# Kernel tuning notes

Measured on AMD Instinct MI355X. Metric: run time of the kernel, lower is better.

Reference implementation:

```python
import jax, jax.numpy as jnp
import numpy as np

B, N, IN_F = 16, 1024, 256
HEADS, OUT_F = 4, 64
NEG_SLOPE = 0.2
CLAMP_MIN = -1e9
MASK_VAL = -9e15


def setup_inputs() -> dict:
    key = jax.random.key(0)
    k1, k2, k3, k4 = jax.random.split(key, 4)
    x = jax.random.normal(k1, (B, N, IN_F), dtype=jnp.float32)
    adj = jax.random.randint(k2, (B, N, N), 0, 2, dtype=jnp.int32)
    # Linear weight, stored as (in, heads*out) so y = x @ W (xavier-uniform scale)
    lim_w = float(np.sqrt(6.0 / (IN_F + HEADS * OUT_F)))
    W = jax.random.uniform(k3, (IN_F, HEADS * OUT_F), dtype=jnp.float32,
                           minval=-lim_w, maxval=lim_w)
    lim_a = float(np.sqrt(6.0 / (2 * OUT_F + HEADS)))
    a = jax.random.uniform(k4, (2 * OUT_F, HEADS), dtype=jnp.float32,
                           minval=-lim_a, maxval=lim_a)
    return {"x": x, "adj": adj, "W": W, "a": a}


def reference(x, adj, W, a):
    Bs, Ns, _ = x.shape
    # Projection: (B,N,H,D)
    h = (x @ W).reshape(Bs, Ns, HEADS, OUT_F)
    # cat([h_i, h_j]) . a == h_i . a_src + h_j . a_dst  (exact same math, no O(N^2*2D) tensor)
    a_src, a_dst = a[:OUT_F], a[OUT_F:]          # each (D, H)
    s_src = jnp.einsum('bnhd,dh->bnh', h, a_src)  # score contribution of node i
    s_dst = jnp.einsum('bnhd,dh->bnh', h, a_dst)  # score contribution of node j
    e = jax.nn.leaky_relu(s_src[:, :, None, :] + s_dst[:, None, :, :],
                          negative_slope=NEG_SLOPE)  # (B,N,N,H)
    # match original: subtract unmasked row max, clamp, then mask, then softmax over j
    e = e - jnp.max(e, axis=2, keepdims=True)
    e = jnp.maximum(e, CLAMP_MIN)
    att = jnp.where(adj[..., None] > 0, e, MASK_VAL)
    att = jax.nn.softmax(att, axis=2)
    h_prime = jnp.einsum('bijh,bjhd->bihd', att, h)  # (B,N,H,D)
    return h_prime.reshape(Bs, Ns, HEADS * OUT_F)
```

## Files before the change

### kernel.cpp

```cpp
#include <hip/hip_runtime.h>
#include <hip/hip_bf16.h>

#define B_   16
#define N_   1024
#define INF_ 256
#define NH_  4
#define HD_  256
#define L2E  1.4426950408889634f

typedef __attribute__((ext_vector_type(8))) short short8;
typedef __attribute__((ext_vector_type(4))) float f32x4;

__device__ __forceinline__ float bf2f(unsigned short u) {
    union { unsigned int i; float f; } v; v.i = ((unsigned int)u) << 16; return v.f;
}
__device__ __forceinline__ unsigned short f2bf(float f) {
    union { float f; unsigned int i; } v; v.f = f;
    unsigned int x = v.i;
    return (unsigned short)((x + 0x7fffu + ((x >> 16) & 1u)) >> 16);
}

__global__ __launch_bounds__(256) void k_prepw(const float* __restrict__ W,
                                               unsigned short* __restrict__ wswz)
{
    int slot = blockIdx.x * 256 + threadIdx.x;
    int kstep = slot >> 10;
    int nt    = (slot >> 6) & 15;
    int lane  = slot & 63;
    int k0 = kstep * 32 + (lane >> 4) * 8;
    int n  = nt * 16 + (lane & 15);
    ushort4 o0, o1;
    o0.x = f2bf(W[(k0 + 0) * HD_ + n]);
    o0.y = f2bf(W[(k0 + 1) * HD_ + n]);
    o0.z = f2bf(W[(k0 + 2) * HD_ + n]);
    o0.w = f2bf(W[(k0 + 3) * HD_ + n]);
    o1.x = f2bf(W[(k0 + 4) * HD_ + n]);
    o1.y = f2bf(W[(k0 + 5) * HD_ + n]);
    o1.z = f2bf(W[(k0 + 6) * HD_ + n]);
    o1.w = f2bf(W[(k0 + 7) * HD_ + n]);
    *(ushort4*)&wswz[(long)slot * 8]     = o0;
    *(ushort4*)&wswz[(long)slot * 8 + 4] = o1;
}

__global__ __launch_bounds__(256) void k_gemm_h(
    const float* __restrict__ x, const float* __restrict__ a,
    const unsigned short* __restrict__ wswz,
    unsigned short* __restrict__ hswz,
    float* __restrict__ ssrc, float* __restrict__ sdst)
{
    __shared__ unsigned short xls[16][264];
    int t = threadIdx.x;
    int blk = blockIdx.x;
    int row0 = blk * 16;
    int b  = blk >> 6;
    int n0 = row0 & 1023;

    {
        int sr = t >> 4, sc = (t & 15) * 16;
        const float* xp = x + (long)(row0 + sr) * INF_ + sc;
        float4 v0 = ((const float4*)xp)[0];
        float4 v1 = ((const float4*)xp)[1];
        float4 v2 = ((const float4*)xp)[2];
        float4 v3 = ((const float4*)xp)[3];
        ushort4 u0 = {f2bf(v0.x), f2bf(v0.y), f2bf(v0.z), f2bf(v0.w)};
        ushort4 u1 = {f2bf(v1.x), f2bf(v1.y), f2bf(v1.z), f2bf(v1.w)};
        ushort4 u2 = {f2bf(v2.x), f2bf(v2.y), f2bf(v2.z), f2bf(v2.w)};
        ushort4 u3 = {f2bf(v3.x), f2bf(v3.y), f2bf(v3.z), f2bf(v3.w)};
        *(ushort4*)&xls[sr][sc]      = u0;
        *(ushort4*)&xls[sr][sc + 4]  = u1;
        *(ushort4*)&xls[sr][sc + 8]  = u2;
        *(ushort4*)&xls[sr][sc + 12] = u3;
    }
    __syncthreads();

    int wave = t >> 6, lane = t & 63, quad = lane >> 4, l15 = lane & 15;
    f32x4 acc[4];
    #pragma unroll
    for (int i = 0; i < 4; i++) acc[i] = (f32x4){0.f, 0.f, 0.f, 0.f};

    #pragma unroll
    for (int ks = 0; ks < 8; ks++) {
        short8 af = *(const short8*)&xls[l15][ks * 32 + quad * 8];
        #pragma unroll
        for (int nt = 0; nt < 4; nt++) {
            short8 bf = *(const short8*)(wswz +
                ((long)((ks * 16 + wave * 4 + nt) * 64 + lane)) * 8);
            acc[nt] = __builtin_amdgcn_mfma_f32_16x16x32_bf16(af, bf, acc[nt], 0, 0, 0);
        }
    }

    int q0 = (quad & 1) * 4;
    int qd = ((row0 & 31) + quad * 4) >> 3;
    long bj32 = row0 >> 5;
    #pragma unroll
    for (int nt = 0; nt < 4; nt++) {
        int dg = wave * 4 + nt;
        long idx8 = (bj32 * 16 + dg) * 64 + qd * 16 + l15;
        ushort4 o = {f2bf(acc[nt][0]), f2bf(acc[nt][1]),
                     f2bf(acc[nt][2]), f2bf(acc[nt][3])};
        *(ushort4*)&hswz[idx8 * 8 + q0] = o;
    }

    float as_[4], ad_[4];
    #pragma unroll
    for (int nt = 0; nt < 4; nt++) {
        int d = nt * 16 + l15;
        as_[nt] = a[d * NH_ + wave];
        ad_[nt] = a[(64 + d) * NH_ + wave];
    }
    #pragma unroll
    for (int r = 0; r < 4; r++) {
        float ps = acc[0][r] * as_[0] + acc[1][r] * as_[1]
                 + acc[2][r] * as_[2] + acc[3][r] * as_[3];
        float pd = acc[0][r] * ad_[0] + acc[1][r] * ad_[1]
                 + acc[2][r] * ad_[2] + acc[3][r] * ad_[3];
        #pragma unroll
        for (int m = 1; m < 16; m <<= 1) {
            ps += __shfl_xor(ps, m);
            pd += __shfl_xor(pd, m);
        }
        if (l15 == 0) {
            int row = n0 + quad * 4 + r;
            ssrc[((long)b * NH_ + wave) * N_ + row] = ps;
            sdst[((long)b * NH_ + wave) * N_ + row] = pd;
        }
    }
}

__global__ __launch_bounds__(256) void k_maxdst(const float* __restrict__ sdst,
                                                float* __restrict__ mx)
{
    int bh = blockIdx.x;
    int t  = threadIdx.x;
    const float* p = sdst + (long)bh * N_;
    float m = -1e30f;
    for (int i = t; i < N_; i += 256) m = fmaxf(m, p[i]);
    #pragma unroll
    for (int s = 1; s < 64; s <<= 1) m = fmaxf(m, __shfl_xor(m, s));
    __shared__ float sm[4];
    if ((t & 63) == 0) sm[t >> 6] = m;
    __syncthreads();
    if (t == 0) mx[bh] = fmaxf(fmaxf(sm[0], sm[1]), fmaxf(sm[2], sm[3]));
}

__global__ __launch_bounds__(512) void k_attn(
    const int* __restrict__ adj, const unsigned short* __restrict__ hswz,
    const float* __restrict__ ssrc, const float* __restrict__ sdst,
    const float* __restrict__ mxd, float* __restrict__ out)
{
    __shared__ float ss_s[4][32], m_s[4][32], den_l[4][32];

    int t = threadIdx.x;
    int b     = blockIdx.x >> 5;
    int itile = blockIdx.x & 31;
    int i0 = itile * 32;
    int wave = t >> 6, lane = t & 63, quad = lane >> 4, l15 = lane & 15;
    int hh = wave & 3, it = wave >> 2;

    if (t < 128) {
        int h = t >> 5, i = t & 31;
        float ss = ssrc[((long)b * NH_ + h) * N_ + i0 + i] * L2E;
        float mxv = mxd[b * NH_ + h] * L2E;
        ss_s[h][i] = ss;
        float e = ss + mxv;
        m_s[h][i] = fmaxf(e, 0.2f * e);
    }
    __syncthreads();

    int irow = it * 16 + l15;
    float ssi = ss_s[hh][irow];
    float mi  = m_s[hh][irow];
    const float* sdp = sdst + ((long)b * NH_ + hh) * N_;
    const int* adjrow = adj + ((long)b * N_ + i0 + irow) * N_;

    f32x4 acc[4];
    #pragma unroll
    for (int i = 0; i < 4; i++) acc[i] = (f32x4){0.f, 0.f, 0.f, 0.f};
    float den = 0.f;

    #pragma unroll 2
    for (int jc = 0; jc < 32; jc++) {
        int j0 = jc * 32;
        float4 s0 = *(const float4*)(sdp + j0 + quad * 8);
        float4 s1 = *(const float4*)(sdp + j0 + quad * 8 + 4);
        int4  a0 = *(const int4*)(adjrow + j0 + quad * 8);
        int4  a1 = *(const int4*)(adjrow + j0 + quad * 8 + 4);
        float sv[8] = {s0.x, s0.y, s0.z, s0.w, s1.x, s1.y, s1.z, s1.w};
        int   av[8] = {a0.x, a0.y, a0.z, a0.w, a1.x, a1.y, a1.z, a1.w};
        short8 af;
        #pragma unroll
        for (int q = 0; q < 8; q++) {
            float e  = ssi + sv[q] * L2E;
            float lr = fmaxf(e, 0.2f * e);
            float w  = (av[q] > 0) ? __builtin_exp2f(lr - mi) : 0.f;
            unsigned short ub = f2bf(w);
            den += bf2f(ub);
            af[q] = (short)ub;
        }
        long base8 = ((long)(b * 32) + jc) * 1024;
        #pragma unroll
        for (int idt = 0; idt < 4; idt++) {
            int dg = hh * 4 + idt;
            short8 bf = *(const short8*)(hswz + (base8 + dg * 64 + lane) * 8);
            acc[idt] = __builtin_amdgcn_mfma_f32_16x16x32_bf16(af, bf, acc[idt], 0, 0, 0);
        }
    }

    den += __shfl_xor(den, 16);
    den += __shfl_xor(den, 32);
    if (quad == 0) den_l[hh][irow] = den;
    __syncthreads();

    #pragma unroll
    for (int idt = 0; idt < 4; idt++) {
        #pragma unroll
        for (int r = 0; r < 4; r++) {
            int ir = it * 16 + quad * 4 + r;
            float inv = 1.0f / den_l[hh][ir];
            out[((long)b * N_ + i0 + ir) * HD_ + hh * 64 + idt * 16 + l15] =
                acc[idt][r] * inv;
        }
    }
}

extern "C" void kernel_launch(void* const* d_in, const int* in_sizes, int n_in,
                              void* d_out, int out_size, void* d_ws, size_t ws_size,
                              hipStream_t stream) {
    const float* x   = (const float*)d_in[0];
    const int*   adj = (const int*)d_in[1];
    const float* W   = (const float*)d_in[2];
    const float* a   = (const float*)d_in[3];
    float* out = (float*)d_out;

    unsigned short* hswz = (unsigned short*)d_ws;
    unsigned short* wswz = hswz + (long)B_ * N_ * HD_;
    float* ssrc = (float*)(wswz + INF_ * HD_);
    float* sdst = ssrc + (long)B_ * NH_ * N_;
    float* mxd  = sdst + (long)B_ * NH_ * N_;

    k_prepw<<<32, 256, 0, stream>>>(W, wswz);
    k_gemm_h<<<1024, 256, 0, stream>>>(x, a, wswz, hswz, ssrc, sdst);
    k_maxdst<<<64, 256, 0, stream>>>(sdst, mxd);
    k_attn<<<512, 512, 0, stream>>>(adj, hswz, ssrc, sdst, mxd, out);
}
```

Before: 176.0 us.

## Split attention over j halves, bit-pack adjacency, drop row-max pass

Adds a kernel that packs the int32 adjacency matrix into bitmasks. The attention kernel then reads one mask word per lane instead of int4 loads inside the loop. The attention kernel uses 16-row tiles with the j range split across two wave groups, and the partial accumulators are merged through shared memory. This doubles the block count to improve parallelism. The max-over-destination kernel and the max subtraction are removed, on the basis that softmax is shift-invariant, and the log2(e) scaling is folded into the projection kernel. The projection GEMM now keeps the W fragments in registers and processes two row tiles per block with a swizzled LDS layout. Without the max shift, exp2 can overflow if scores are large, and the packing kernel still reads the whole adjacency matrix.

```diff
diff --git a/kernel.cpp b/kernel.cpp
--- a/kernel.cpp
+++ b/kernel.cpp
@@ -42,64 +42,55 @@
     *(ushort4*)&wswz[(long)slot * 8 + 4] = o1;
 }
 
-__global__ __launch_bounds__(256) void k_gemm_h(
+__global__ __launch_bounds__(256) void k_pack(const int* __restrict__ adj,
+                                              unsigned int* __restrict__ pb)
+{
+    int g = blockIdx.x * 256 + threadIdx.x;
+    int gw   = g & 7;
+    int lane = (g >> 3) & 63;
+    int it   = (g >> 9) & 63;
+    int b    = g >> 15;
+    int row  = it * 16 + (lane & 15);
+    int quad = lane >> 4;
+    const int* ar = adj + ((long)(b * N_ + row) << 10);
+    unsigned int u = 0;
+    #pragma unroll
+    for (int jl = 0; jl < 4; jl++) {
+        int j0 = (gw * 4 + jl) * 32 + quad * 8;
+        int4 a0 = *(const int4*)(ar + j0);
+        int4 a1 = *(const int4*)(ar + j0 + 4);
+        u |= ((unsigned)a0.x) << (jl * 8 + 0);
+        u |= ((unsigned)a0.y) << (jl * 8 + 1);
+        u |= ((unsigned)a0.z) << (jl * 8 + 2);
+        u |= ((unsigned)a0.w) << (jl * 8 + 3);
+        u |= ((unsigned)a1.x) << (jl * 8 + 4);
+        u |= ((unsigned)a1.y) << (jl * 8 + 5);
+        u |= ((unsigned)a1.z) << (jl * 8 + 6);
+        u |= ((unsigned)a1.w) << (jl * 8 + 7);
+    }
+    pb[g] = u;
+}
+
+__global__ __launch_bounds__(256, 2) void k_gemm_h(
     const float* __restrict__ x, const float* __restrict__ a,
     const unsigned short* __restrict__ wswz,
     unsigned short* __restrict__ hswz,
     float* __restrict__ ssrc, float* __restrict__ sdst)
 {
-    __shared__ unsigned short xls[16][264];
+    __shared__ unsigned short xf[2][4096];
     int t = threadIdx.x;
-    int blk = blockIdx.x;
-    int row0 = blk * 16;
-    int b  = blk >> 6;
-    int n0 = row0 & 1023;
-
-    {
-        int sr = t >> 4, sc = (t & 15) * 16;
-        const float* xp = x + (long)(row0 + sr) * INF_ + sc;
-        float4 v0 = ((const float4*)xp)[0];
-        float4 v1 = ((const float4*)xp)[1];
-        float4 v2 = ((const float4*)xp)[2];
-        float4 v3 = ((const float4*)xp)[3];
-        ushort4 u0 = {f2bf(v0.x), f2bf(v0.y), f2bf(v0.z), f2bf(v0.w)};
-        ushort4 u1 = {f2bf(v1.x), f2bf(v1.y), f2bf(v1.z), f2bf(v1.w)};
-        ushort4 u2 = {f2bf(v2.x), f2bf(v2.y), f2bf(v2.z), f2bf(v2.w)};
-        ushort4 u3 = {f2bf(v3.x), f2bf(v3.y), f2bf(v3.z), f2bf(v3.w)};
-        *(ushort4*)&xls[sr][sc]      = u0;
-        *(ushort4*)&xls[sr][sc + 4]  = u1;
-        *(ushort4*)&xls[sr][sc + 8]  = u2;
-        *(ushort4*)&xls[sr][sc + 12] = u3;
-    }
-    __syncthreads();
-
     int wave = t >> 6, lane = t & 63, quad = lane >> 4, l15 = lane & 15;
-    f32x4 acc[4];
-    #pragma unroll
-    for (int i = 0; i < 4; i++) acc[i] = (f32x4){0.f, 0.f, 0.f, 0.f};
-
-    #pragma unroll
-    for (int ks = 0; ks < 8; ks++) {
-        short8 af = *(const short8*)&xls[l15][ks * 32 + quad * 8];
-        #pragma unroll
-        for (int nt = 0; nt < 4; nt++) {
-            short8 bf = *(const short8*)(wswz +
+
+    short8 bw[8][4];
+    #pragma unroll
+    for (int ks = 0; ks < 8; ks++)
+        #pragma unroll
+        for (int nt = 0; nt < 4; nt++)
+            bw[ks][nt] = *(const short8*)(wswz +
                 ((long)((ks * 16 + wave * 4 + nt) * 64 + lane)) * 8);
-            acc[nt] = __builtin_amdgcn_mfma_f32_16x16x32_bf16(af, bf, acc[nt], 0, 0, 0);
-        }
-    }
-
-    int q0 = (quad & 1) * 4;
-    int qd = ((row0 & 31) + quad * 4) >> 3;
-    long bj32 = row0 >> 5;
-    #pragma unroll
-    for (int nt = 0; nt < 4; nt++) {
-        int dg = wave * 4 + nt;
-        long idx8 = (bj32 * 16 + dg) * 64 + qd * 16 + l15;
-        ushort4 o = {f2bf(acc[nt][0]), f2bf(acc[nt][1]),
-                     f2bf(acc[nt][2]), f2bf(acc[nt][3])};
-        *(ushort4*)&hswz[idx8 * 8 + q0] = o;
-    }
+
+    int sr = t >> 4, c = t & 15;
+    int ks0 = c >> 1, qA = (c & 1) * 2;
 
     float as_[4], ad_[4];
     #pragma unroll
@@ -108,117 +99,169 @@
         as_[nt] = a[d * NH_ + wave];
         ad_[nt] = a[(64 + d) * NH_ + wave];
     }
-    #pragma unroll
-    for (int r = 0; r < 4; r++) {
-        float ps = acc[0][r] * as_[0] + acc[1][r] * as_[1]
-                 + acc[2][r] * as_[2] + acc[3][r] * as_[3];
-        float pd = acc[0][r] * ad_[0] + acc[1][r] * ad_[1]
-                 + acc[2][r] * ad_[2] + acc[3][r] * ad_[3];
-        #pragma unroll
-        for (int m = 1; m < 16; m <<= 1) {
-            ps += __shfl_xor(ps, m);
-            pd += __shfl_xor(pd, m);
-        }
-        if (l15 == 0) {
-            int row = n0 + quad * 4 + r;
-            ssrc[((long)b * NH_ + wave) * N_ + row] = ps;
-            sdst[((long)b * NH_ + wave) * N_ + row] = pd;
-        }
-    }
-}
-
-__global__ __launch_bounds__(256) void k_maxdst(const float* __restrict__ sdst,
-                                                float* __restrict__ mx)
-{
-    int bh = blockIdx.x;
+
+    for (int s = 0; s < 2; s++) {
+        int row0 = (blockIdx.x * 2 + s) * 16;
+        int b  = row0 >> 10;
+        int n0 = row0 & 1023;
+        unsigned short* xb = &xf[s][0];
+
+        {
+            const float* xp = x + (long)(row0 + sr) * INF_ + c * 16;
+            float4 v0 = ((const float4*)xp)[0];
+            float4 v1 = ((const float4*)xp)[1];
+            float4 v2 = ((const float4*)xp)[2];
+            float4 v3 = ((const float4*)xp)[3];
+            short8 u0, u1;
+            u0[0] = (short)f2bf(v0.x); u0[1] = (short)f2bf(v0.y);
+            u0[2] = (short)f2bf(v0.z); u0[3] = (short)f2bf(v0.w);
+            u0[4] = (short)f2bf(v1.x); u0[5] = (short)f2bf(v1.y);
+            u0[6] = (short)f2bf(v1.z); u0[7] = (short)f2bf(v1.w);
+            u1[0] = (short)f2bf(v2.x); u1[1] = (short)f2bf(v2.y);
+            u1[2] = (short)f2bf(v2.z); u1[3] = (short)f2bf(v2.w);
+            u1[4] = (short)f2bf(v3.x); u1[5] = (short)f2bf(v3.y);
+            u1[6] = (short)f2bf(v3.z); u1[7] = (short)f2bf(v3.w);
+            int sw = (ks0 & 1) << 2;
+            int i1 = ks0 * 64 + (((qA    ) * 16 + sr) ^ sw);
+            int i2 = ks0 * 64 + (((qA + 1) * 16 + sr) ^ sw);
+            *(short8*)(xb + i1 * 8) = u0;
+            *(short8*)(xb + i2 * 8) = u1;
+        }
+        __syncthreads();
+
+        f32x4 acc[4];
+        #pragma unroll
+        for (int i = 0; i < 4; i++) acc[i] = (f32x4){0.f, 0.f, 0.f, 0.f};
+
+        #pragma unroll
+        for (int ks = 0; ks < 8; ks++) {
+            short8 af = *(const short8*)(xb +
+                (ks * 64 + (lane ^ ((ks & 1) << 2))) * 8);
+            #pragma unroll
+            for (int nt = 0; nt < 4; nt++)
+                acc[nt] = __builtin_amdgcn_mfma_f32_16x16x32_bf16(af, bw[ks][nt], acc[nt], 0, 0, 0);
+        }
+
+        int q0 = (quad & 1) * 4;
+        int qd = ((row0 & 31) >> 3) + (quad >> 1);
+        long bj32 = row0 >> 5;
+        #pragma unroll
+        for (int nt = 0; nt < 4; nt++) {
+            int dg = wave * 4 + nt;
+            long idx8 = (bj32 * 16 + dg) * 64 + qd * 16 + l15;
+            ushort4 o = {f2bf(acc[nt][0]), f2bf(acc[nt][1]),
+                         f2bf(acc[nt][2]), f2bf(acc[nt][3])};
+            *(ushort4*)&hswz[idx8 * 8 + q0] = o;
+        }
+
+        #pragma unroll
+        for (int r = 0; r < 4; r++) {
+            float ps = acc[0][r] * as_[0] + acc[1][r] * as_[1]
+                     + acc[2][r] * as_[2] + acc[3][r] * as_[3];
+            float pd = acc[0][r] * ad_[0] + acc[1][r] * ad_[1]
+                     + acc[2][r] * ad_[2] + acc[3][r] * ad_[3];
+            #pragma unroll
+            for (int m = 1; m < 16; m <<= 1) {
+                ps += __shfl_xor(ps, m);
+                pd += __shfl_xor(pd, m);
+            }
+            if (l15 == 0) {
+                int row = n0 + quad * 4 + r;
+                ssrc[((long)b * NH_ + wave) * N_ + row] = ps * L2E;
+                sdst[((long)b * NH_ + wave) * N_ + row] = pd * L2E;
+            }
+        }
+    }
+}
+
+__global__ __launch_bounds__(512, 6) void k_attn(
+    const unsigned int* __restrict__ pb, const unsigned short* __restrict__ hswz,
+    const float* __restrict__ ssrc, const float* __restrict__ sdst,
+    float* __restrict__ out)
+{
+    __shared__ float ss_s[4][16];
+    __shared__ float accb[4][64][20];
+    __shared__ float denb[4][64];
+
     int t  = threadIdx.x;
-    const float* p = sdst + (long)bh * N_;
-    float m = -1e30f;
-    for (int i = t; i < N_; i += 256) m = fmaxf(m, p[i]);
-    #pragma unroll
-    for (int s = 1; s < 64; s <<= 1) m = fmaxf(m, __shfl_xor(m, s));
-    __shared__ float sm[4];
-    if ((t & 63) == 0) sm[t >> 6] = m;
+    int bx = blockIdx.x;
+    int b  = bx >> 6, it = bx & 63;
+    int i0 = it * 16;
+    int wave = t >> 6, lane = t & 63, quad = lane >> 4, l15 = lane & 15;
+    int hh = wave & 3, jh = wave >> 2;
+
+    if (t < 64) {
+        int h = t >> 4, i = t & 15;
+        ss_s[h][i] = ssrc[((long)(b * NH_ + h)) * N_ + i0 + i];
+    }
     __syncthreads();
-    if (t == 0) mx[bh] = fmaxf(fmaxf(sm[0], sm[1]), fmaxf(sm[2], sm[3]));
-}
-
-__global__ __launch_bounds__(512) void k_attn(
-    const int* __restrict__ adj, const unsigned short* __restrict__ hswz,
-    const float* __restrict__ ssrc, const float* __restrict__ sdst,
-    const float* __restrict__ mxd, float* __restrict__ out)
-{
-    __shared__ float ss_s[4][32], m_s[4][32], den_l[4][32];
-
-    int t = threadIdx.x;
-    int b     = blockIdx.x >> 5;
-    int itile = blockIdx.x & 31;
-    int i0 = itile * 32;
-    int wave = t >> 6, lane = t & 63, quad = lane >> 4, l15 = lane & 15;
-    int hh = wave & 3, it = wave >> 2;
-
-    if (t < 128) {
-        int h = t >> 5, i = t & 31;
-        float ss = ssrc[((long)b * NH_ + h) * N_ + i0 + i] * L2E;
-        float mxv = mxd[b * NH_ + h] * L2E;
-        ss_s[h][i] = ss;
-        float e = ss + mxv;
-        m_s[h][i] = fmaxf(e, 0.2f * e);
-    }
-    __syncthreads();
-
-    int irow = it * 16 + l15;
-    float ssi = ss_s[hh][irow];
-    float mi  = m_s[hh][irow];
-    const float* sdp = sdst + ((long)b * NH_ + hh) * N_;
-    const int* adjrow = adj + ((long)b * N_ + i0 + irow) * N_;
+
+    float ssi = ss_s[hh][l15];
+    const float* sdp = sdst + ((long)(b * NH_ + hh)) * N_ + jh * 512;
+    uint4 mr = *(const uint4*)(pb + ((long)((b * 64 + it) * 64 + lane)) * 8 + jh * 4);
 
     f32x4 acc[4];
     #pragma unroll
     for (int i = 0; i < 4; i++) acc[i] = (f32x4){0.f, 0.f, 0.f, 0.f};
     float den = 0.f;
 
-    #pragma unroll 2
-    for (int jc = 0; jc < 32; jc++) {
-        int j0 = jc * 32;
-        float4 s0 = *(const float4*)(sdp + j0 + quad * 8);
-        float4 s1 = *(const float4*)(sdp + j0 + quad * 8 + 4);
-        int4  a0 = *(const int4*)(adjrow + j0 + quad * 8);
-        int4  a1 = *(const int4*)(adjrow + j0 + quad * 8 + 4);
+    #pragma unroll 4
+    for (int jc = 0; jc < 16; jc++) {
+        unsigned int mwd = (jc & 8) ? ((jc & 4) ? mr.w : mr.z)
+                                    : ((jc & 4) ? mr.y : mr.x);
+        unsigned int byv = (mwd >> ((jc & 3) * 8)) & 0xffu;
+
+        const float* sj = sdp + jc * 32 + quad * 8;
+        float4 s0 = *(const float4*)sj;
+        float4 s1 = *(const float4*)(sj + 4);
         float sv[8] = {s0.x, s0.y, s0.z, s0.w, s1.x, s1.y, s1.z, s1.w};
-        int   av[8] = {a0.x, a0.y, a0.z, a0.w, a1.x, a1.y, a1.z, a1.w};
+
         short8 af;
         #pragma unroll
         for (int q = 0; q < 8; q++) {
-            float e  = ssi + sv[q] * L2E;
+            float e  = ssi + sv[q];
             float lr = fmaxf(e, 0.2f * e);
-            float w  = (av[q] > 0) ? __builtin_exp2f(lr - mi) : 0.f;
+            float w  = __builtin_exp2f(lr);
+            w = ((byv >> q) & 1u) ? w : 0.0f;
             unsigned short ub = f2bf(w);
             den += bf2f(ub);
             af[q] = (short)ub;
         }
-        long base8 = ((long)(b * 32) + jc) * 1024;
+
+        long s8 = ((long)(b * 32 + jh * 16 + jc)) * 16 * 64;
         #pragma unroll
         for (int idt = 0; idt < 4; idt++) {
             int dg = hh * 4 + idt;
-            short8 bf = *(const short8*)(hswz + (base8 + dg * 64 + lane) * 8);
+            short8 bf = *(const short8*)(hswz + (s8 + dg * 64 + lane) * 8);
             acc[idt] = __builtin_amdgcn_mfma_f32_16x16x32_bf16(af, bf, acc[idt], 0, 0, 0);
         }
     }
 
-    den += __shfl_xor(den, 16);
-    den += __shfl_xor(den, 32);
-    if (quad == 0) den_l[hh][irow] = den;
+    if (jh == 1) {
+        #pragma unroll
+        for (int idt = 0; idt < 4; idt++)
+            *(f32x4*)&accb[hh][lane][idt * 4] = acc[idt];
+        denb[hh][lane] = den;
+    }
     __syncthreads();
 
-    #pragma unroll
-    for (int idt = 0; idt < 4; idt++) {
-        #pragma unroll
-        for (int r = 0; r < 4; r++) {
-            int ir = it * 16 + quad * 4 + r;
-            float inv = 1.0f / den_l[hh][ir];
-            out[((long)b * N_ + i0 + ir) * HD_ + hh * 64 + idt * 16 + l15] =
-                acc[idt][r] * inv;
+    if (jh == 0) {
+        den += denb[hh][lane];
+        den += __shfl_xor(den, 16);
+        den += __shfl_xor(den, 32);
+        float dv[4];
+        #pragma unroll
+        for (int r = 0; r < 4; r++)
+            dv[r] = 1.0f / __shfl(den, quad * 4 + r);
+        #pragma unroll
+        for (int idt = 0; idt < 4; idt++) {
+            f32x4 other = *(const f32x4*)&accb[hh][lane][idt * 4];
+            #pragma unroll
+            for (int r = 0; r < 4; r++) {
+                int irow = i0 + quad * 4 + r;
+                out[((long)(b * N_ + irow)) * HD_ + hh * 64 + idt * 16 + l15] =
+                    (acc[idt][r] + other[r]) * dv[r];
+            }
         }
     }
 }
@@ -232,14 +275,14 @@
     const float* a   = (const float*)d_in[3];
     float* out = (float*)d_out;
 
-    unsigned short* hswz = (unsigned short*)d_ws;
-    unsigned short* wswz = hswz + (long)B_ * N_ * HD_;
+    unsigned int* pb      = (unsigned int*)d_ws;
+    unsigned short* hswz  = (unsigned short*)(pb + 524288);
+    unsigned short* wswz  = hswz + (long)B_ * N_ * HD_;
     float* ssrc = (float*)(wswz + INF_ * HD_);
     float* sdst = ssrc + (long)B_ * NH_ * N_;
-    float* mxd  = sdst + (long)B_ * NH_ * N_;
 
     k_prepw<<<32, 256, 0, stream>>>(W, wswz);
-    k_gemm_h<<<1024, 256, 0, stream>>>(x, a, wswz, hswz, ssrc, sdst);
-    k_maxdst<<<64, 256, 0, stream>>>(sdst, mxd);
-    k_attn<<<512, 512, 0, stream>>>(adj, hswz, ssrc, sdst, mxd, out);
-}
+    k_pack<<<2048, 256, 0, stream>>>(adj, pb);
+    k_gemm_h<<<512, 256, 0, stream>>>(x, a, wswz, hswz, ssrc, sdst);
+    k_attn<<<1024, 512, 0, stream>>>(pb, hswz, ssrc, sdst, out);
+}
```

New measurement: 175.5 us. No clear change (-0.3%).

## Bit-pack adjacency, split j across waves, reuse B tiles, drop max pass

Applied to the files above, without the earlier changes.

Adds a prep stage that packs the int32 adjacency matrix into bitmasks, fused with the W swizzle. The attention kernel changes so each wave handles two 16-row tiles over half of the j range, reusing every loaded h fragment for two MFMAs. The two j-halves are combined through shared memory, and the row-sum denominator is computed with an MFMA against a ones vector. The separate max-reduction kernel is removed and the log2(e) scale is folded into the GEMM epilogue. The exponent is no longer shifted by a row maximum, so overflow safety now depends on the score range.

```diff
diff --git a/kernel.cpp b/kernel.cpp
--- a/kernel.cpp
+++ b/kernel.cpp
@@ -20,26 +20,46 @@
     return (unsigned short)((x + 0x7fffu + ((x >> 16) & 1u)) >> 16);
 }
 
-__global__ __launch_bounds__(256) void k_prepw(const float* __restrict__ W,
-                                               unsigned short* __restrict__ wswz)
+__global__ __launch_bounds__(256) void k_prep(const int* __restrict__ adj,
+                                              const float* __restrict__ W,
+                                              unsigned int* __restrict__ pb,
+                                              unsigned short* __restrict__ wswz)
 {
-    int slot = blockIdx.x * 256 + threadIdx.x;
-    int kstep = slot >> 10;
-    int nt    = (slot >> 6) & 15;
-    int lane  = slot & 63;
-    int k0 = kstep * 32 + (lane >> 4) * 8;
-    int n  = nt * 16 + (lane & 15);
-    ushort4 o0, o1;
-    o0.x = f2bf(W[(k0 + 0) * HD_ + n]);
-    o0.y = f2bf(W[(k0 + 1) * HD_ + n]);
-    o0.z = f2bf(W[(k0 + 2) * HD_ + n]);
-    o0.w = f2bf(W[(k0 + 3) * HD_ + n]);
-    o1.x = f2bf(W[(k0 + 4) * HD_ + n]);
-    o1.y = f2bf(W[(k0 + 5) * HD_ + n]);
-    o1.z = f2bf(W[(k0 + 6) * HD_ + n]);
-    o1.w = f2bf(W[(k0 + 7) * HD_ + n]);
-    *(ushort4*)&wswz[(long)slot * 8]     = o0;
-    *(ushort4*)&wswz[(long)slot * 8 + 4] = o1;
+    int bx = blockIdx.x, t = threadIdx.x;
+    if (bx < 2048) {
+        int wave = t >> 6, lane = t & 63;
+        int row = bx * 8 + wave * 2 + (lane >> 5);
+        int w   = lane & 31;
+        const int4* ar = (const int4*)(adj + ((long)row << 10) + w * 32);
+        unsigned int u = 0;
+        #pragma unroll
+        for (int k = 0; k < 8; k++) {
+            int4 a = ar[k];
+            u |= ((unsigned)a.x) << (4 * k);
+            u |= ((unsigned)a.y) << (4 * k + 1);
+            u |= ((unsigned)a.z) << (4 * k + 2);
+            u |= ((unsigned)a.w) << (4 * k + 3);
+        }
+        pb[((long)row << 5) + w] = u;
+    } else {
+        int slot = (bx - 2048) * 256 + t;
+        int kstep = slot >> 10;
+        int nt    = (slot >> 6) & 15;
+        int lane  = slot & 63;
+        int k0 = kstep * 32 + (lane >> 4) * 8;
+        int n  = nt * 16 + (lane & 15);
+        ushort4 o0, o1;
+        o0.x = f2bf(W[(k0 + 0) * HD_ + n]);
+        o0.y = f2bf(W[(k0 + 1) * HD_ + n]);
+        o0.z = f2bf(W[(k0 + 2) * HD_ + n]);
+        o0.w = f2bf(W[(k0 + 3) * HD_ + n]);
+        o1.x = f2bf(W[(k0 + 4) * HD_ + n]);
+        o1.y = f2bf(W[(k0 + 5) * HD_ + n]);
+        o1.z = f2bf(W[(k0 + 6) * HD_ + n]);
+        o1.w = f2bf(W[(k0 + 7) * HD_ + n]);
+        *(ushort4*)&wswz[(long)slot * 8]     = o0;
+        *(ushort4*)&wswz[(long)slot * 8 + 4] = o1;
+    }
 }
 
 __global__ __launch_bounds__(256) void k_gemm_h(
@@ -121,104 +141,124 @@
         }
         if (l15 == 0) {
             int row = n0 + quad * 4 + r;
-            ssrc[((long)b * NH_ + wave) * N_ + row] = ps;
-            sdst[((long)b * NH_ + wave) * N_ + row] = pd;
-        }
-    }
-}
-
-__global__ __launch_bounds__(256) void k_maxdst(const float* __restrict__ sdst,
-                                                float* __restrict__ mx)
+            ssrc[((long)b * NH_ + wave) * N_ + row] = ps * L2E;
+            sdst[((long)b * NH_ + wave) * N_ + row] = pd * L2E;
+        }
+    }
+}
+
+__global__ __launch_bounds__(512, 4) void k_attn(
+    const unsigned int* __restrict__ pb, const unsigned short* __restrict__ hswz,
+    const float* __restrict__ ssrc, const float* __restrict__ sdst,
+    float* __restrict__ out)
 {
-    int bh = blockIdx.x;
-    int t  = threadIdx.x;
-    const float* p = sdst + (long)bh * N_;
-    float m = -1e30f;
-    for (int i = t; i < N_; i += 256) m = fmaxf(m, p[i]);
-    #pragma unroll
-    for (int s = 1; s < 64; s <<= 1) m = fmaxf(m, __shfl_xor(m, s));
-    __shared__ float sm[4];
-    if ((t & 63) == 0) sm[t >> 6] = m;
-    __syncthreads();
-    if (t == 0) mx[bh] = fmaxf(fmaxf(sm[0], sm[1]), fmaxf(sm[2], sm[3]));
-}
-
-__global__ __launch_bounds__(512) void k_attn(
-    const int* __restrict__ adj, const unsigned short* __restrict__ hswz,
-    const float* __restrict__ ssrc, const float* __restrict__ sdst,
-    const float* __restrict__ mxd, float* __restrict__ out)
-{
-    __shared__ float ss_s[4][32], m_s[4][32], den_l[4][32];
+    __shared__ float ss_s[4][32];
+    __shared__ float accb[4][2][64][20];
 
     int t = threadIdx.x;
-    int b     = blockIdx.x >> 5;
-    int itile = blockIdx.x & 31;
-    int i0 = itile * 32;
+    int b  = blockIdx.x >> 5, ig = blockIdx.x & 31;
+    int i0 = ig * 32;
     int wave = t >> 6, lane = t & 63, quad = lane >> 4, l15 = lane & 15;
-    int hh = wave & 3, it = wave >> 2;
+    int hh = wave & 3, jh = wave >> 2;
 
     if (t < 128) {
         int h = t >> 5, i = t & 31;
-        float ss = ssrc[((long)b * NH_ + h) * N_ + i0 + i] * L2E;
-        float mxv = mxd[b * NH_ + h] * L2E;
-        ss_s[h][i] = ss;
-        float e = ss + mxv;
-        m_s[h][i] = fmaxf(e, 0.2f * e);
+        ss_s[h][i] = ssrc[((long)(b * NH_ + h)) * N_ + i0 + i];
     }
     __syncthreads();
 
-    int irow = it * 16 + l15;
-    float ssi = ss_s[hh][irow];
-    float mi  = m_s[hh][irow];
-    const float* sdp = sdst + ((long)b * NH_ + hh) * N_;
-    const int* adjrow = adj + ((long)b * N_ + i0 + irow) * N_;
-
-    f32x4 acc[4];
-    #pragma unroll
-    for (int i = 0; i < 4; i++) acc[i] = (f32x4){0.f, 0.f, 0.f, 0.f};
-    float den = 0.f;
-
-    #pragma unroll 2
-    for (int jc = 0; jc < 32; jc++) {
-        int j0 = jc * 32;
-        float4 s0 = *(const float4*)(sdp + j0 + quad * 8);
-        float4 s1 = *(const float4*)(sdp + j0 + quad * 8 + 4);
-        int4  a0 = *(const int4*)(adjrow + j0 + quad * 8);
-        int4  a1 = *(const int4*)(adjrow + j0 + quad * 8 + 4);
-        float sv[8] = {s0.x, s0.y, s0.z, s0.w, s1.x, s1.y, s1.z, s1.w};
-        int   av[8] = {a0.x, a0.y, a0.z, a0.w, a1.x, a1.y, a1.z, a1.w};
-        short8 af;
-        #pragma unroll
-        for (int q = 0; q < 8; q++) {
-            float e  = ssi + sv[q] * L2E;
-            float lr = fmaxf(e, 0.2f * e);
-            float w  = (av[q] > 0) ? __builtin_exp2f(lr - mi) : 0.f;
-            unsigned short ub = f2bf(w);
-            den += bf2f(ub);
-            af[q] = (short)ub;
-        }
-        long base8 = ((long)(b * 32) + jc) * 1024;
+    float ss0 = ss_s[hh][l15];
+    float ss1 = ss_s[hh][16 + l15];
+    const float* sdp = sdst + ((long)(b * NH_ + hh)) * N_ + jh * 512;
+    long grow0 = ((long)b << 10) + i0 + l15;
+    const unsigned int* pb0 = pb + (grow0 << 5) + jh * 16;
+    const unsigned int* pb1 = pb0 + (16 << 5);
+
+    f32x4 acc0[4], acc1[4], dn0, dn1;
+    #pragma unroll
+    for (int i = 0; i < 4; i++) {
+        acc0[i] = (f32x4){0.f, 0.f, 0.f, 0.f};
+        acc1[i] = (f32x4){0.f, 0.f, 0.f, 0.f};
+    }
+    dn0 = (f32x4){0.f, 0.f, 0.f, 0.f};
+    dn1 = (f32x4){0.f, 0.f, 0.f, 0.f};
+    short8 ones;
+    #pragma unroll
+    for (int i = 0; i < 8; i++) ones[i] = (short)0x3F80;
+
+    int shq = quad * 8;
+
+    #pragma unroll 4
+    for (int jc = 0; jc < 16; jc++) {
+        unsigned int m0 = (pb0[jc] >> shq) & 0xffu;
+        unsigned int m1 = (pb1[jc] >> shq) & 0xffu;
+        const float* sj = sdp + jc * 32 + quad * 8;
+        float4 sA = *(const float4*)sj;
+        float4 sB = *(const float4*)(sj + 4);
+        float sv[8] = {sA.x, sA.y, sA.z, sA.w, sB.x, sB.y, sB.z, sB.w};
+
+        union { unsigned int u[4]; short8 s; } p0, p1;
+        #pragma unroll
+        for (int qp = 0; qp < 4; qp++) {
+            unsigned int wb[2][2];
+            #pragma unroll
+            for (int hv = 0; hv < 2; hv++) {
+                int q = 2 * qp + hv;
+                float e0 = ss0 + sv[q];
+                float w0 = __builtin_exp2f(fmaxf(e0, 0.2f * e0));
+                w0 = ((m0 >> q) & 1u) ? w0 : 0.f;
+                float e1 = ss1 + sv[q];
+                float w1 = __builtin_exp2f(fmaxf(e1, 0.2f * e1));
+                w1 = ((m1 >> q) & 1u) ? w1 : 0.f;
+                wb[0][hv] = __float_as_uint(w0) + 0x8000u;
+                wb[1][hv] = __float_as_uint(w1) + 0x8000u;
+            }
+            p0.u[qp] = (wb[0][1] & 0xffff0000u) | (wb[0][0] >> 16);
+            p1.u[qp] = (wb[1][1] & 0xffff0000u) | (wb[1][0] >> 16);
+        }
+
+        long s8 = ((long)(b * 32 + jh * 16 + jc)) * 1024;
         #pragma unroll
         for (int idt = 0; idt < 4; idt++) {
-            int dg = hh * 4 + idt;
-            short8 bf = *(const short8*)(hswz + (base8 + dg * 64 + lane) * 8);
-            acc[idt] = __builtin_amdgcn_mfma_f32_16x16x32_bf16(af, bf, acc[idt], 0, 0, 0);
-        }
-    }
-
-    den += __shfl_xor(den, 16);
-    den += __shfl_xor(den, 32);
-    if (quad == 0) den_l[hh][irow] = den;
+            short8 bf = *(const short8*)(hswz + (s8 + (hh * 4 + idt) * 64 + lane) * 8);
+            acc0[idt] = __builtin_amdgcn_mfma_f32_16x16x32_bf16(p0.s, bf, acc0[idt], 0, 0, 0);
+            acc1[idt] = __builtin_amdgcn_mfma_f32_16x16x32_bf16(p1.s, bf, acc1[idt], 0, 0, 0);
+        }
+        dn0 = __builtin_amdgcn_mfma_f32_16x16x32_bf16(p0.s, ones, dn0, 0, 0, 0);
+        dn1 = __builtin_amdgcn_mfma_f32_16x16x32_bf16(p1.s, ones, dn1, 0, 0, 0);
+    }
+
+    if (jh == 1) {
+        #pragma unroll
+        for (int idt = 0; idt < 4; idt++) {
+            *(f32x4*)&accb[hh][0][lane][idt * 4] = acc0[idt];
+            *(f32x4*)&accb[hh][1][lane][idt * 4] = acc1[idt];
+        }
+        *(f32x4*)&accb[hh][0][lane][16] = dn0;
+        *(f32x4*)&accb[hh][1][lane][16] = dn1;
+    }
     __syncthreads();
 
-    #pragma unroll
-    for (int idt = 0; idt < 4; idt++) {
+    if (jh == 0) {
+        f32x4 od0 = *(const f32x4*)&accb[hh][0][lane][16];
+        f32x4 od1 = *(const f32x4*)&accb[hh][1][lane][16];
+        float inv0[4], inv1[4];
         #pragma unroll
         for (int r = 0; r < 4; r++) {
-            int ir = it * 16 + quad * 4 + r;
-            float inv = 1.0f / den_l[hh][ir];
-            out[((long)b * N_ + i0 + ir) * HD_ + hh * 64 + idt * 16 + l15] =
-                acc[idt][r] * inv;
+            inv0[r] = 1.0f / (dn0[r] + od0[r]);
+            inv1[r] = 1.0f / (dn1[r] + od1[r]);
+        }
+        #pragma unroll
+        for (int idt = 0; idt < 4; idt++) {
+            f32x4 o0 = *(const f32x4*)&accb[hh][0][lane][idt * 4];
+            f32x4 o1 = *(const f32x4*)&accb[hh][1][lane][idt * 4];
+            int col = hh * 64 + idt * 16 + l15;
+            #pragma unroll
+            for (int r = 0; r < 4; r++) {
+                long row_g = (long)b * N_ + i0 + quad * 4 + r;
+                out[row_g * HD_ + col] = (acc0[idt][r] + o0[r]) * inv0[r];
+                out[(row_g + 16) * HD_ + col] = (acc1[idt][r] + o1[r]) * inv1[r];
+            }
         }
     }
 }
@@ -232,14 +272,13 @@
     const float* a   = (const float*)d_in[3];
     float* out = (float*)d_out;
 
-    unsigned short* hswz = (unsigned short*)d_ws;
-    unsigned short* wswz = hswz + (long)B_ * N_ * HD_;
+    unsigned int* pb      = (unsigned int*)d_ws;
+    unsigned short* hswz  = (unsigned short*)(pb + 524288);
+    unsigned short* wswz  = hswz + (long)B_ * N_ * HD_;
     float* ssrc = (float*)(wswz + INF_ * HD_);
     float* sdst = ssrc + (long)B_ * NH_ * N_;
-    float* mxd  = sdst + (long)B_ * NH_ * N_;
-
-    k_prepw<<<32, 256, 0, stream>>>(W, wswz);
+
+    k_prep<<<2080, 256, 0, stream>>>(adj, W, pb, wswz);
     k_gemm_h<<<1024, 256, 0, stream>>>(x, a, wswz, hswz, ssrc, sdst);
-    k_maxdst<<<64, 256, 0, stream>>>(sdst, mxd);
-    k_attn<<<512, 512, 0, stream>>>(adj, hswz, ssrc, sdst, mxd, out);
-}
+    k_attn<<<512, 512, 0, stream>>>(pb, hswz, ssrc, sdst, out);
+}
```

Result: faster. 156.0 us (-11.4%).
